# Performance work log

Measured on AMD Instinct MI355X. Metric: run time of the kernel, lower is better.

Reference implementation:

```python
import jax, jax.numpy as jnp
import numpy as np

KERNEL_NUM = 21
SIGMA = 0.1
EXACT_SIGMA = 0.001

def _kernel_params():
    mus, sigs = [], []
    for i in range(KERNEL_NUM):
        mu = 1.0 / (KERNEL_NUM - 1) + 2.0 * i / (KERNEL_NUM - 1) - 1.0
        s = SIGMA
        if mu > 1:
            mu = 1.0
            s = EXACT_SIGMA
        mus.append(mu)
        sigs.append(s)
    return np.array(mus, np.float32), np.array(sigs, np.float32)

MUS, SIGS = _kernel_params()

def _l2norm(x):
    # torch F.normalize(p=2, dim=-1): x / max(||x||, 1e-12)
    n = jnp.sqrt(jnp.sum(x * x, axis=-1, keepdims=True))
    return x / jnp.maximum(n, 1e-12)

def setup_inputs() -> dict:
    key = jax.random.key(0)
    ks = jax.random.split(key, 8)
    B, W, R, D, V = 512, 30, 512, 128, 100000
    H1, H2 = 128, 64
    return {
        "query": jax.random.randint(ks[0], (B, W), 0, V),
        "document": jax.random.randint(ks[1], (B, R), 0, V),
        "emb_table": jax.random.normal(ks[2], (V, D), jnp.float32) * 0.02,
        "w1": jax.random.normal(ks[3], (KERNEL_NUM, H1), jnp.float32) * 0.1,
        "b1": jnp.zeros((H1,), jnp.float32),
        "w2": jax.random.normal(ks[4], (H1, H2), jnp.float32) * 0.1,
        "b2": jnp.zeros((H2,), jnp.float32),
        "w3": jax.random.normal(ks[5], (H2, 1), jnp.float32) * 0.1,
        "b3": jnp.zeros((1,), jnp.float32),
    }

def reference(query, document, emb_table, w1, b1, w2, b2, w3, b3):
    q = _l2norm(emb_table[query])      # [B, W, D]
    d = _l2norm(emb_table[document])   # [B, R, D]
    # cosine matching matrix [B, W, R]
    M = jnp.einsum('bwd,brd->bwr', q, d)
    # 21 Gaussian soft-histogram bins: log1p(sum_{w,r} exp(-0.5*(M-mu)^2/sigma^2))
    KM = [
        jnp.log1p(
            jnp.sum(jnp.exp(-0.5 * (M - MUS[i]) ** 2 / (SIGS[i] ** 2)), axis=(-1, -2))
        )
        for i in range(KERNEL_NUM)
    ]
    k = jnp.stack(KM, axis=1)  # [B, K]
    h = jax.nn.relu(k @ w1 + b1)
    h = jax.nn.relu(h @ w2 + b2)
    return h @ w3 + b3  # [B, 1]
```

## Files before the change

kernel.cpp:

```cpp
#include <hip/hip_runtime.h>
#include <math.h>

#define B_   512
#define W_   30
#define R_   512
#define D_   128
#define NK_  21
#define SPLIT 4
#define QSTRIDE 132

typedef __attribute__((ext_vector_type(8))) short  bf16x8;
typedef __attribute__((ext_vector_type(4))) float  f32x4;
typedef __attribute__((ext_vector_type(2))) float  f32x2;

__device__ __forceinline__ unsigned short f2bf(float f) {
    union { float f; unsigned int u; } v; v.f = f;
    unsigned int u = v.u;
    return (unsigned short)((u + 0x7fffu + ((u >> 16) & 1u)) >> 16);
}

__device__ __forceinline__ float fast_exp2(float x) {
#if __has_builtin(__builtin_amdgcn_exp2f)
    return __builtin_amdgcn_exp2f(x);
#else
    float r; asm volatile("v_exp_f32 %0, %1" : "=v"(r) : "v"(x)); return r;
#endif
}

#define QROWS 32
#define QST   136

__global__ __launch_bounds__(512) void knrm_bins_kernel(
    const int* __restrict__ query, const int* __restrict__ doc,
    const float* __restrict__ emb,
    float* __restrict__ part)
{
    const int bid  = blockIdx.x;
    const int b    = bid >> 2;
    const int sp   = bid & 3;
    const int tid  = threadIdx.x;
    const int lane = tid & 63;
    const int wid  = tid >> 6;
    const int l15  = lane & 15;
    const int lhi  = lane >> 4;

    __shared__ unsigned short qlds[QROWS * QST];
    __shared__ float wred[8][NK_];

    const int di = doc[b * R_ + sp * 128 + wid * 16 + l15];
    const float* drow = emb + (size_t)di * D_ + lhi * 8;
    float4 f[8];
    #pragma unroll
    for (int kk = 0; kk < 4; ++kk) {
        f[2 * kk]     = *(const float4*)(drow + kk * 32);
        f[2 * kk + 1] = *(const float4*)(drow + kk * 32 + 4);
    }

    {
        int w = tid >> 4, j = tid & 15;
        uint4 o4 = make_uint4(0, 0, 0, 0);
        if (w < W_) {
            int qi = query[b * W_ + w];
            const float* qrow = emb + (size_t)qi * D_ + j * 8;
            float4 qa = *(const float4*)(qrow);
            float4 qb = *(const float4*)(qrow + 4);
            float ss = qa.x*qa.x + qa.y*qa.y + qa.z*qa.z + qa.w*qa.w
                     + qb.x*qb.x + qb.y*qb.y + qb.z*qb.z + qb.w*qb.w;
            #pragma unroll
            for (int off = 8; off >= 1; off >>= 1) ss += __shfl_xor(ss, off, 16);
            float qinv = 1.0f / fmaxf(sqrtf(ss), 1e-12f);
            unsigned short o[8];
            o[0] = f2bf(qa.x*qinv); o[1] = f2bf(qa.y*qinv);
            o[2] = f2bf(qa.z*qinv); o[3] = f2bf(qa.w*qinv);
            o[4] = f2bf(qb.x*qinv); o[5] = f2bf(qb.y*qinv);
            o[6] = f2bf(qb.z*qinv); o[7] = f2bf(qb.w*qinv);
            o4 = *(const uint4*)o;
        }
        *(uint4*)(&qlds[(tid >> 4) * QST + (tid & 15) * 8]) = o4;
    }

    float nsq = 0.f;
    #pragma unroll
    for (int c = 0; c < 8; ++c)
        nsq = fmaf(f[c].x, f[c].x, fmaf(f[c].y, f[c].y,
              fmaf(f[c].z, f[c].z, fmaf(f[c].w, f[c].w, nsq))));
    nsq += __shfl_xor(nsq, 16, 64);
    nsq += __shfl_xor(nsq, 32, 64);
    const float dinv = 1.0f / fmaxf(sqrtf(nsq), 1e-12f);

    bf16x8 a[4];
    #pragma unroll
    for (int kk = 0; kk < 4; ++kk) {
        float4 u = f[2 * kk], v = f[2 * kk + 1];
        unsigned short o[8];
        o[0] = f2bf(u.x*dinv); o[1] = f2bf(u.y*dinv);
        o[2] = f2bf(u.z*dinv); o[3] = f2bf(u.w*dinv);
        o[4] = f2bf(v.x*dinv); o[5] = f2bf(v.y*dinv);
        o[6] = f2bf(v.z*dinv); o[7] = f2bf(v.w*dinv);
        a[kk] = *(const bf16x8*)o;
    }
    __syncthreads();

    bf16x8 bq[2][4];
    #pragma unroll
    for (int tc = 0; tc < 2; ++tc)
        #pragma unroll
        for (int kk = 0; kk < 4; ++kk)
            bq[tc][kk] = *(const bf16x8*)&qlds[(tc * 16 + l15) * QST + kk * 32 + lhi * 8];

    f32x4 acc0 = (f32x4)0.0f, acc1 = (f32x4)0.0f;
    #pragma unroll
    for (int kk = 0; kk < 4; ++kk) {
        acc0 = __builtin_amdgcn_mfma_f32_16x16x32_bf16(a[kk], bq[0][kk], acc0, 0, 0, 0);
        acc1 = __builtin_amdgcn_mfma_f32_16x16x32_bf16(a[kk], bq[1][kk], acc1, 0, 0, 0);
    }

    const float CW = -72.134752f;
    const float CE = -721347.52f;

    f32x2 kacc2[NK_];
    #pragma unroll
    for (int i = 0; i < NK_; ++i) kacc2[i] = (f32x2)0.0f;

    #pragma unroll
    for (int p = 0; p < 4; ++p) {
        f32x2 mm;
        mm.x = acc0[p];
        mm.y = (l15 < 14) ? acc1[p] : 3.0f;
        f32x2 t = mm + 0.95f;
        f32x2 e = (CW * t) * t;
        f32x2 d = 14.4269504f * t - 0.72134752f;
        #pragma unroll
        for (int i = 0; i < 20; ++i) {
            f32x2 T;
            T.x = fast_exp2(e.x);
            T.y = fast_exp2(e.y);
            kacc2[i] += T;
            e += d;
            d += -1.44269504f;
        }
        f32x2 y = mm - 1.0f;
        f32x2 a20 = (CE * y) * y;
        f32x2 T20;
        T20.x = fast_exp2(a20.x);
        T20.y = fast_exp2(a20.y);
        kacc2[20] += T20;
    }

    #pragma unroll
    for (int i = 0; i < NK_; ++i) {
        float v = kacc2[i].x + kacc2[i].y;
        #pragma unroll
        for (int off = 32; off >= 1; off >>= 1) v += __shfl_xor(v, off, 64);
        if (lane == 0) wred[wid][i] = v;
    }
    __syncthreads();
    if (tid < NK_) {
        float s = 0.f;
        #pragma unroll
        for (int ww = 0; ww < 8; ++ww) s += wred[ww][tid];
        part[bid * NK_ + tid] = s;
    }
}

__global__ __launch_bounds__(128) void knrm_mlp_kernel(
    const float* __restrict__ part,
    const float* __restrict__ w1, const float* __restrict__ b1,
    const float* __restrict__ w2, const float* __restrict__ b2,
    const float* __restrict__ w3, const float* __restrict__ b3,
    float* __restrict__ out)
{
    const int b   = blockIdx.x;
    const int tid = threadIdx.x;

    __shared__ float klds[NK_];
    __shared__ float h1lds[128];

    if (tid < NK_) {
        const float* p0 = part + (size_t)b * SPLIT * NK_;
        float s = p0[tid] + p0[NK_ + tid] + p0[2 * NK_ + tid] + p0[3 * NK_ + tid];
        klds[tid] = log1pf(s);
    }
    __syncthreads();

    {
        float h = b1[tid];
        #pragma unroll
        for (int i = 0; i < NK_; ++i) h = fmaf(klds[i], w1[i * 128 + tid], h);
        h1lds[tid] = fmaxf(h, 0.f);
    }
    __syncthreads();

    if (tid < 64) {
        float h = b2[tid];
        #pragma unroll 8
        for (int i = 0; i < 128; ++i) h = fmaf(h1lds[i], w2[i * 64 + tid], h);
        float p = fmaxf(h, 0.f) * w3[tid];
        #pragma unroll
        for (int off = 32; off >= 1; off >>= 1) p += __shfl_xor(p, off, 64);
        if (tid == 0) out[b] = p + b3[0];
    }
}

__global__ __launch_bounds__(512) void knrm_kernel(
    const int* __restrict__ query, const int* __restrict__ doc,
    const float* __restrict__ emb,
    const float* __restrict__ w1, const float* __restrict__ b1,
    const float* __restrict__ w2, const float* __restrict__ b2,
    const float* __restrict__ w3, const float* __restrict__ b3,
    float* __restrict__ out)
{
    const int b   = blockIdx.x;
    const int tid = threadIdx.x;

    __shared__ float qs[W_ * QSTRIDE];
    __shared__ float qinv[W_];
    __shared__ float wred[8][NK_];
    __shared__ float klds[NK_];
    __shared__ float h1lds[128];

    for (int idx = tid; idx < W_ * D_; idx += 512) {
        int w = idx >> 7, k = idx & 127;
        int qi = query[b * W_ + w];
        qs[w * QSTRIDE + k] = emb[(size_t)qi * D_ + k];
    }
    __syncthreads();

    if (tid < W_ * 16) {
        int row = tid >> 4, j = tid & 15;
        float ss = 0.f;
        #pragma unroll
        for (int k = 0; k < D_; k += 16) {
            float v = qs[row * QSTRIDE + k + j];
            ss = fmaf(v, v, ss);
        }
        #pragma unroll
        for (int off = 8; off >= 1; off >>= 1) ss += __shfl_xor(ss, off, 16);
        if (j == 0) qinv[row] = 1.0f / fmaxf(sqrtf(ss), 1e-12f);
    }
    __syncthreads();

    const int didx = doc[b * R_ + tid];
    const float4* __restrict__ drow = (const float4*)(emb + (size_t)didx * D_);

    float acc[W_];
    #pragma unroll
    for (int w = 0; w < W_; ++w) acc[w] = 0.f;
    float nsq = 0.f;

    float4 dv = drow[0];
    for (int c = 0; c < D_ / 4; ++c) {
        float4 dnx = drow[(c + 1) & 31];
        nsq = fmaf(dv.x, dv.x, fmaf(dv.y, dv.y, fmaf(dv.z, dv.z, fmaf(dv.w, dv.w, nsq))));
        const float* qc = qs + c * 4;
        #pragma unroll
        for (int w = 0; w < W_; ++w) {
            float4 qv = *(const float4*)(qc + w * QSTRIDE);
            acc[w] = fmaf(qv.x, dv.x, fmaf(qv.y, dv.y, fmaf(qv.z, dv.z, fmaf(qv.w, dv.w, acc[w]))));
        }
        dv = dnx;
    }
    const float invd = 1.0f / fmaxf(sqrtf(nsq), 1e-12f);

    const float CW = -72.134752f;
    const float CE = -721347.52f;
    float kacc[NK_];
    #pragma unroll
    for (int i = 0; i < NK_; ++i) kacc[i] = 0.f;

    #pragma unroll
    for (int w = 0; w < W_; ++w) {
        float m = acc[w] * qinv[w] * invd;
        #pragma unroll
        for (int i = 0; i < 20; ++i) {
            const float mu = (float)(1.0 / (NK_ - 1) + 2.0 * (double)i / (NK_ - 1) - 1.0);
            float t = m - mu;
            kacc[i] += exp2f(CW * t * t);
        }
        float y = m - 1.0f;
        kacc[20] += exp2f(CE * y * y);
    }

    const int wid = tid >> 6, lane = tid & 63;
    #pragma unroll
    for (int i = 0; i < NK_; ++i) {
        float v = kacc[i];
        #pragma unroll
        for (int off = 32; off >= 1; off >>= 1) v += __shfl_xor(v, off, 64);
        if (lane == 0) wred[wid][i] = v;
    }
    __syncthreads();
    if (tid < NK_) {
        float s = 0.f;
        #pragma unroll
        for (int ww = 0; ww < 8; ++ww) s += wred[ww][tid];
        klds[tid] = log1pf(s);
    }
    __syncthreads();

    if (tid < 128) {
        float h = b1[tid];
        #pragma unroll
        for (int i = 0; i < NK_; ++i) h = fmaf(klds[i], w1[i * 128 + tid], h);
        h1lds[tid] = fmaxf(h, 0.f);
    }
    __syncthreads();
    if (tid < 64) {
        float h = b2[tid];
        #pragma unroll 8
        for (int i = 0; i < 128; ++i) h = fmaf(h1lds[i], w2[i * 64 + tid], h);
        float p = fmaxf(h, 0.f) * w3[tid];
        #pragma unroll
        for (int off = 32; off >= 1; off >>= 1) p += __shfl_xor(p, off, 64);
        if (tid == 0) out[b] = p + b3[0];
    }
}

extern "C" void kernel_launch(void* const* d_in, const int* in_sizes, int n_in,
                              void* d_out, int out_size, void* d_ws, size_t ws_size,
                              hipStream_t stream) {
    const int*   query = (const int*)d_in[0];
    const int*   doc   = (const int*)d_in[1];
    const float* emb   = (const float*)d_in[2];
    const float* w1    = (const float*)d_in[3];
    const float* b1    = (const float*)d_in[4];
    const float* w2    = (const float*)d_in[5];
    const float* b2    = (const float*)d_in[6];
    const float* w3    = (const float*)d_in[7];
    const float* b3    = (const float*)d_in[8];
    float* outp = (float*)d_out;

    const size_t part_bytes = (size_t)B_ * SPLIT * NK_ * sizeof(float);

    if (ws_size >= part_bytes) {
        float* part = (float*)d_ws;
        knrm_bins_kernel<<<dim3(B_ * SPLIT), dim3(512), 0, stream>>>(query, doc, emb, part);
        knrm_mlp_kernel<<<dim3(B_), dim3(128), 0, stream>>>(part, w1, b1, w2, b2, w3, b3, outp);
    } else {
        knrm_kernel<<<dim3(B_), dim3(512), 0, stream>>>(query, doc, emb,
                                                        w1, b1, w2, b2, w3, b3, outp);
    }
}
```

Measured before the change: 52.13 us.

## Compute Gaussian bins via geometric recurrence, shorten wave reduction, remap block order

The 20 per-element exp2 calls for the Gaussian bins are replaced by three groups, each seeded with two exp2 values and then advanced by multiplicative recurrence (R*=r, r*=e^-1). This trades transcendental throughput for multiplies. Risks are float drift or underflow across up to seven steps, which the regrouping is meant to bound. The cross-lane reduction now does only three shuffles and finishes with an 8-way sum from LDS. Block IDs are remapped so neighbouring blocks work on different batches, with the partial-result index adjusted to match.

```diff
diff --git a/kernel.cpp b/kernel.cpp
--- a/kernel.cpp
+++ b/kernel.cpp
@@ -36,8 +36,8 @@
     float* __restrict__ part)
 {
     const int bid  = blockIdx.x;
-    const int b    = bid >> 2;
-    const int sp   = bid & 3;
+    const int b    = ((bid >> 5) << 3) | (bid & 7);
+    const int sp   = (bid >> 3) & 3;
     const int tid  = threadIdx.x;
     const int lane = tid & 63;
     const int wid  = tid >> 6;
@@ -45,7 +45,7 @@
     const int lhi  = lane >> 4;
 
     __shared__ unsigned short qlds[QROWS * QST];
-    __shared__ float wred[8][NK_];
+    __shared__ float wred8[8][NK_][8];
 
     const int di = doc[b * R_ + sp * 128 + wid * 16 + l15];
     const float* drow = emb + (size_t)di * D_ + lhi * 8;
@@ -117,6 +117,7 @@
 
     const float CW = -72.134752f;
     const float CE = -721347.52f;
+    const float RC = 0.36787944f;
 
     f32x2 kacc2[NK_];
     #pragma unroll
@@ -127,18 +128,29 @@
         f32x2 mm;
         mm.x = acc0[p];
         mm.y = (l15 < 14) ? acc1[p] : 3.0f;
-        f32x2 t = mm + 0.95f;
-        f32x2 e = (CW * t) * t;
-        f32x2 d = 14.4269504f * t - 0.72134752f;
-        #pragma unroll
-        for (int i = 0; i < 20; ++i) {
-            f32x2 T;
-            T.x = fast_exp2(e.x);
-            T.y = fast_exp2(e.y);
-            kacc2[i] += T;
-            e += d;
-            d += -1.44269504f;
-        }
+        f32x2 t0 = mm + 0.95f;
+
+        #pragma unroll
+        for (int g = 0; g < 3; ++g) {
+            const int   gs = (g == 0) ? 0 : (g == 1) ? 7 : 14;
+            const int   gl = (g == 2) ? 6 : 7;
+            const float go = 0.1f * (float)gs;
+            f32x2 tg = t0 - go;
+            f32x2 e  = (CW * tg) * tg;
+            f32x2 dl = 14.4269504f * tg - 0.72134752f;
+            f32x2 R, r;
+            R.x = fast_exp2(e.x);  R.y = fast_exp2(e.y);
+            r.x = fast_exp2(dl.x); r.y = fast_exp2(dl.y);
+            #pragma unroll
+            for (int k = 0; k < 7; ++k) {
+                if (k < gl) {
+                    kacc2[gs + k] += R;
+                    R *= r;
+                    r *= RC;
+                }
+            }
+        }
+
         f32x2 y = mm - 1.0f;
         f32x2 a20 = (CE * y) * y;
         f32x2 T20;
@@ -150,16 +162,19 @@
     #pragma unroll
     for (int i = 0; i < NK_; ++i) {
         float v = kacc2[i].x + kacc2[i].y;
-        #pragma unroll
-        for (int off = 32; off >= 1; off >>= 1) v += __shfl_xor(v, off, 64);
-        if (lane == 0) wred[wid][i] = v;
+        v += __shfl_xor(v, 8, 64);
+        v += __shfl_xor(v, 16, 64);
+        v += __shfl_xor(v, 32, 64);
+        if (lane < 8) wred8[wid][i][lane] = v;
     }
     __syncthreads();
     if (tid < NK_) {
         float s = 0.f;
         #pragma unroll
-        for (int ww = 0; ww < 8; ++ww) s += wred[ww][tid];
-        part[bid * NK_ + tid] = s;
+        for (int ww = 0; ww < 8; ++ww)
+            #pragma unroll
+            for (int c = 0; c < 8; ++c) s += wred8[ww][tid][c];
+        part[(b * SPLIT + sp) * NK_ + tid] = s;
     }
 }
 
```

Result: faster. 42.69 us (-18.1%).
